# Kernel optimization log

Measured on AMD Instinct MI355X. Metric: run time of the kernel, lower is better.

Reference implementation:

```python
import jax, jax.numpy as jnp
import numpy as np

INPUT_SIZE = 350   # (133 + 42) * 2
HIDDEN = 2048

def setup_inputs() -> dict:
    key = jax.random.key(0)
    ks = jax.random.split(key, 11)
    s = 0.02
    H4 = 4 * HIDDEN
    return {
        "x":     jax.random.normal(ks[0], (1, 133, 2), jnp.float32),
        "W_ih0": jax.random.normal(ks[1], (H4, INPUT_SIZE), jnp.float32) * s,
        "W_hh0": jax.random.normal(ks[2], (H4, HIDDEN), jnp.float32) * s,
        "b_ih0": jax.random.normal(ks[3], (H4,), jnp.float32) * s,
        "b_hh0": jax.random.normal(ks[4], (H4,), jnp.float32) * s,
        "W_ih1": jax.random.normal(ks[5], (H4, HIDDEN), jnp.float32) * s,
        "W_hh1": jax.random.normal(ks[6], (H4, HIDDEN), jnp.float32) * s,
        "b_ih1": jax.random.normal(ks[7], (H4,), jnp.float32) * s,
        "b_hh1": jax.random.normal(ks[8], (H4,), jnp.float32) * s,
        "fc_w":  jax.random.normal(ks[9], (INPUT_SIZE, HIDDEN), jnp.float32) * s,
        "fc_b":  jax.random.normal(ks[10], (INPUT_SIZE,), jnp.float32) * s,
    }

def _prepare(x):
    kp = x[0].astype(jnp.float32)                 # [133, 2]
    src_body, src_face = kp[0], kp[53]
    src_left, src_right = kp[100], kp[121]
    body = kp[:17] - src_body
    feet = kp[17:23]                              # never recentered in original
    face = kp[23:91] - src_face
    l0, r0 = kp[91:112], kp[112:133]
    # bounding-box scales computed BEFORE recentering (matches torch order)
    wl = l0[:, 0].max() - l0[:, 0].min(); hl = l0[:, 1].max() - l0[:, 1].min()
    wr = r0[:, 0].max() - r0[:, 0].min(); hr = r0[:, 1].max() - r0[:, 1].min()
    chin2l = l0 - src_body
    chin2r = r0 - src_body
    left = l0 - src_left
    right = r0 - src_right
    okl = (wl != 0.0) & (hl != 0.0)
    okr = (wr != 0.0) & (hr != 0.0)
    dl = jnp.where(okl, jnp.stack([wl, hl]), jnp.ones(2, kp.dtype))
    dr = jnp.where(okr, jnp.stack([wr, hr]), jnp.ones(2, kp.dtype))
    left = left / dl
    right = right / dr
    return jnp.concatenate([body, feet, face, left, right, chin2l, chin2r]).reshape(INPUT_SIZE)

def _lstm_cell(xin, h, c, Wih, Whh, bih, bhh):
    g = Wih @ xin + bih + Whh @ h + bhh           # [4H]
    i, f, gg, o = jnp.split(g, 4)                 # PyTorch gate order i,f,g,o
    c_new = jax.nn.sigmoid(f) * c + jax.nn.sigmoid(i) * jnp.tanh(gg)
    h_new = jax.nn.sigmoid(o) * jnp.tanh(c_new)
    return h_new, c_new

def reference(x, W_ih0, W_hh0, b_ih0, b_hh0, W_ih1, W_hh1, b_ih1, b_hh1, fc_w, fc_b):
    feat = _prepare(x)                            # [350]
    h0 = jnp.zeros(HIDDEN, feat.dtype)            # initialize_cell_and_hidden_state
    c0 = jnp.zeros(HIDDEN, feat.dtype)
    h1, _ = _lstm_cell(feat, h0, c0, W_ih0, W_hh0, b_ih0, b_hh0)
    h2, _ = _lstm_cell(h1, h0, c0, W_ih1, W_hh1, b_ih1, b_hh1)
    return (fc_w @ h2 + fc_b)[None, :]            # [1, 350]
```

## Files before the change

kernel.cpp:

```cpp
#include <hip/hip_runtime.h>
#include <math.h>

#define HIDDEN 2048
#define IN_F 350

__device__ __forceinline__ float sigmoidf_(float v) { return 1.0f / (1.0f + expf(-v)); }

__device__ void compute_feat(const float* __restrict__ x, float* feat) {
    __shared__ float sc[12];
    const int t = threadIdx.x;
    if (t == 0) {
        sc[0] = x[0];   sc[1] = x[1];
        sc[2] = x[106]; sc[3] = x[107];
        sc[4] = x[200]; sc[5] = x[201];
        sc[6] = x[242]; sc[7] = x[243];
        float lminx = x[182], lmaxx = x[182], lminy = x[183], lmaxy = x[183];
        for (int j = 1; j < 21; ++j) {
            float vx = x[182 + 2*j], vy = x[183 + 2*j];
            lminx = fminf(lminx, vx); lmaxx = fmaxf(lmaxx, vx);
            lminy = fminf(lminy, vy); lmaxy = fmaxf(lmaxy, vy);
        }
        float wl = lmaxx - lminx, hl = lmaxy - lminy;
        float rminx = x[224], rmaxx = x[224], rminy = x[225], rmaxy = x[225];
        for (int j = 1; j < 21; ++j) {
            float vx = x[224 + 2*j], vy = x[225 + 2*j];
            rminx = fminf(rminx, vx); rmaxx = fmaxf(rmaxx, vx);
            rminy = fminf(rminy, vy); rmaxy = fmaxf(rmaxy, vy);
        }
        float wr = rmaxx - rminx, hr = rmaxy - rminy;
        bool okl = (wl != 0.0f) && (hl != 0.0f);
        bool okr = (wr != 0.0f) && (hr != 0.0f);
        sc[8]  = okl ? wl : 1.0f;  sc[9]  = okl ? hl : 1.0f;
        sc[10] = okr ? wr : 1.0f;  sc[11] = okr ? hr : 1.0f;
    }
    __syncthreads();
    const float sbx = sc[0], sby = sc[1], sfx = sc[2], sfy = sc[3];
    const float slx = sc[4], sly = sc[5], srx = sc[6], sry = sc[7];
    const float dlx = sc[8], dly = sc[9], drx = sc[10], dry = sc[11];
    for (int k = t; k < 133; k += blockDim.x) {
        float vx = x[2*k], vy = x[2*k + 1];
        if (k < 17) {
            feat[2*k]   = vx - sbx;  feat[2*k+1] = vy - sby;
        } else if (k < 23) {
            feat[2*k]   = vx;        feat[2*k+1] = vy;
        } else if (k < 91) {
            feat[2*k]   = vx - sfx;  feat[2*k+1] = vy - sfy;
        } else if (k < 112) {
            int j = k - 91;
            feat[182 + 2*j] = (vx - slx) / dlx;  feat[183 + 2*j] = (vy - sly) / dly;
            feat[266 + 2*j] = vx - sbx;          feat[267 + 2*j] = vy - sby;
        } else {
            int j = k - 112;
            feat[224 + 2*j] = (vx - srx) / drx;  feat[225 + 2*j] = (vy - sry) / dry;
            feat[308 + 2*j] = vx - sbx;          feat[309 + 2*j] = vy - sby;
        }
    }
    __syncthreads();
}

__global__ __launch_bounds__(192) void lstm0_kernel(
    const float* __restrict__ x, const float* __restrict__ Wih,
    const float* __restrict__ bih, const float* __restrict__ bhh,
    float* __restrict__ h_out)
{
    __shared__ float feat[IN_F];
    __shared__ float gate_s[3];
    compute_feat(x, feat);
    const int j = blockIdx.x;
    const int wave = threadIdx.x >> 6;
    const int lane = threadIdx.x & 63;
    const int gate = (wave == 0) ? 0 : (wave == 1 ? 2 : 3);
    const int row = gate * HIDDEN + j;
    const float* wr = Wih + (size_t)row * IN_F;
    float acc = 0.0f;
    for (int i = lane; i < IN_F; i += 64) acc += wr[i] * feat[i];
    #pragma unroll
    for (int off = 32; off; off >>= 1) acc += __shfl_down(acc, off);
    if (lane == 0) gate_s[wave] = acc + bih[row] + bhh[row];
    __syncthreads();
    if (threadIdx.x == 0) {
        float c = sigmoidf_(gate_s[0]) * tanhf(gate_s[1]);
        h_out[j] = sigmoidf_(gate_s[2]) * tanhf(c);
    }
}

__global__ __launch_bounds__(192) void lstm1_kernel(
    const float* __restrict__ h_in, const float* __restrict__ Wih,
    const float* __restrict__ bih, const float* __restrict__ bhh,
    float* __restrict__ h_out)
{
    __shared__ float gate_s[3];
    const int j = blockIdx.x;
    const int wave = threadIdx.x >> 6;
    const int lane = threadIdx.x & 63;
    const int gate = (wave == 0) ? 0 : (wave == 1 ? 2 : 3);
    const int row = gate * HIDDEN + j;
    const float4* wr4 = (const float4*)(Wih + (size_t)row * HIDDEN);
    const float4* h4  = (const float4*)h_in;
    float acc = 0.0f;
    #pragma unroll
    for (int i = lane; i < HIDDEN / 4; i += 64) {
        float4 w = wr4[i]; float4 v = h4[i];
        acc += w.x * v.x + w.y * v.y + w.z * v.z + w.w * v.w;
    }
    #pragma unroll
    for (int off = 32; off; off >>= 1) acc += __shfl_down(acc, off);
    if (lane == 0) gate_s[wave] = acc + bih[row] + bhh[row];
    __syncthreads();
    if (threadIdx.x == 0) {
        float c = sigmoidf_(gate_s[0]) * tanhf(gate_s[1]);
        h_out[j] = sigmoidf_(gate_s[2]) * tanhf(c);
    }
}

__global__ __launch_bounds__(256) void fc_kernel(
    const float* __restrict__ h_in, const float* __restrict__ W,
    const float* __restrict__ b, float* __restrict__ out)
{
    const int wave = threadIdx.x >> 6;
    const int lane = threadIdx.x & 63;
    const int r = blockIdx.x * 4 + wave;
    if (r >= IN_F) return;
    const float4* wr4 = (const float4*)(W + (size_t)r * HIDDEN);
    const float4* h4  = (const float4*)h_in;
    float acc = 0.0f;
    #pragma unroll
    for (int i = lane; i < HIDDEN / 4; i += 64) {
        float4 w = wr4[i]; float4 v = h4[i];
        acc += w.x * v.x + w.y * v.y + w.z * v.z + w.w * v.w;
    }
    #pragma unroll
    for (int off = 32; off; off >>= 1) acc += __shfl_down(acc, off);
    if (lane == 0) out[r] = acc + b[r];
}

extern "C" void kernel_launch(void* const* d_in, const int* in_sizes, int n_in,
                              void* d_out, int out_size, void* d_ws, size_t ws_size,
                              hipStream_t stream) {
    const float* x     = (const float*)d_in[0];
    const float* W_ih0 = (const float*)d_in[1];
    const float* b_ih0 = (const float*)d_in[3];
    const float* b_hh0 = (const float*)d_in[4];
    const float* W_ih1 = (const float*)d_in[5];
    const float* b_ih1 = (const float*)d_in[7];
    const float* b_hh1 = (const float*)d_in[8];
    const float* fc_w  = (const float*)d_in[9];
    const float* fc_b  = (const float*)d_in[10];

    float* ws = (float*)d_ws;
    float* h1 = ws;
    float* h2 = ws + HIDDEN;

    lstm0_kernel<<<HIDDEN, 192, 0, stream>>>(x, W_ih0, b_ih0, b_hh0, h1);
    lstm1_kernel<<<HIDDEN, 192, 0, stream>>>(h1, W_ih1, b_ih1, b_hh1, h2);
    fc_kernel<<<(IN_F + 3) / 4, 256, 0, stream>>>(h2, fc_w, fc_b, (float*)d_out);
}
```

Before: 22.88 us.

## Parallelize feature prep, unroll GEMV loads, split FC rows across waves

Feature preparation now spreads the hand bounding-box min/max across several threads using shared staging, instead of a serial scan on thread 0. The LSTM0 GEMV is rewritten as fixed float2 loads, and LSTM1 issues all eight float4 weight loads up front to raise memory-level parallelism. The FC kernel now uses one block per output row with four waves splitting the K dimension, which raises the block count from 88 to 350 at the cost of an extra shared-memory reduction and barrier. The float2 loads in LSTM0 assume 8-byte alignment of rows of length 350, which holds because 350 is even.

```diff
diff --git a/kernel.cpp b/kernel.cpp
--- a/kernel.cpp
+++ b/kernel.cpp
@@ -5,39 +5,53 @@
 #define IN_F 350
 
 __device__ __forceinline__ float sigmoidf_(float v) { return 1.0f / (1.0f + expf(-v)); }
+__device__ __forceinline__ float dot4_(float4 a, float4 b) {
+    return a.x*b.x + a.y*b.y + a.z*b.z + a.w*b.w;
+}
 
-__device__ void compute_feat(const float* __restrict__ x, float* feat) {
+__global__ __launch_bounds__(192) void k1_feat_lstm0(
+    const float* __restrict__ x, const float* __restrict__ Wih,
+    const float* __restrict__ bih, const float* __restrict__ bhh,
+    float* __restrict__ h1)
+{
+    __shared__ __align__(16) float feat[IN_F];
+    __shared__ float hx[84];
     __shared__ float sc[12];
-    const int t = threadIdx.x;
-    if (t == 0) {
-        sc[0] = x[0];   sc[1] = x[1];
-        sc[2] = x[106]; sc[3] = x[107];
-        sc[4] = x[200]; sc[5] = x[201];
-        sc[6] = x[242]; sc[7] = x[243];
-        float lminx = x[182], lmaxx = x[182], lminy = x[183], lmaxy = x[183];
-        for (int j = 1; j < 21; ++j) {
-            float vx = x[182 + 2*j], vy = x[183 + 2*j];
-            lminx = fminf(lminx, vx); lmaxx = fmaxf(lmaxx, vx);
-            lminy = fminf(lminy, vy); lmaxy = fmaxf(lmaxy, vy);
-        }
-        float wl = lmaxx - lminx, hl = lmaxy - lminy;
-        float rminx = x[224], rmaxx = x[224], rminy = x[225], rmaxy = x[225];
-        for (int j = 1; j < 21; ++j) {
-            float vx = x[224 + 2*j], vy = x[225 + 2*j];
-            rminx = fminf(rminx, vx); rmaxx = fmaxf(rmaxx, vx);
-            rminy = fminf(rminy, vy); rmaxy = fmaxf(rmaxy, vy);
-        }
-        float wr = rmaxx - rminx, hr = rmaxy - rminy;
-        bool okl = (wl != 0.0f) && (hl != 0.0f);
-        bool okr = (wr != 0.0f) && (hr != 0.0f);
-        sc[8]  = okl ? wl : 1.0f;  sc[9]  = okl ? hl : 1.0f;
-        sc[10] = okr ? wr : 1.0f;  sc[11] = okr ? hr : 1.0f;
+    __shared__ float ext[4];
+    __shared__ float gd[3];
+    const int tid = threadIdx.x, wave = tid >> 6, lane = tid & 63;
+    const int j = blockIdx.x;
+
+    if (tid < 84) hx[tid] = x[182 + tid];
+    else if (tid < 92) {
+        int t = tid - 84;
+        int p = t >> 1;
+        int base = (p == 0) ? 0 : (p == 1) ? 106 : (p == 2) ? 200 : 242;
+        sc[t] = x[base + (t & 1)];
     }
     __syncthreads();
-    const float sbx = sc[0], sby = sc[1], sfx = sc[2], sfy = sc[3];
-    const float slx = sc[4], sly = sc[5], srx = sc[6], sry = sc[7];
-    const float dlx = sc[8], dly = sc[9], drx = sc[10], dry = sc[11];
-    for (int k = t; k < 133; k += blockDim.x) {
+    if (tid < 4) {
+        const int h = tid >> 1, c = tid & 1;
+        float m = hx[h*42 + c], M = m;
+        #pragma unroll
+        for (int jj = 1; jj < 21; ++jj) {
+            float v = hx[h*42 + 2*jj + c];
+            m = fminf(m, v); M = fmaxf(M, v);
+        }
+        ext[tid] = M - m;
+    }
+    __syncthreads();
+    if (tid < 4) {
+        const int h = tid >> 1;
+        bool ok = (ext[2*h] != 0.0f) && (ext[2*h + 1] != 0.0f);
+        sc[8 + tid] = ok ? ext[tid] : 1.0f;
+    }
+    __syncthreads();
+    if (tid < 133) {
+        const float sbx = sc[0], sby = sc[1], sfx = sc[2], sfy = sc[3];
+        const float slx = sc[4], sly = sc[5], srx = sc[6], sry = sc[7];
+        const float dlx = sc[8], dly = sc[9], drx = sc[10], dry = sc[11];
+        const int k = tid;
         float vx = x[2*k], vy = x[2*k + 1];
         if (k < 17) {
             feat[2*k]   = vx - sbx;  feat[2*k+1] = vy - sby;
@@ -46,92 +60,97 @@
         } else if (k < 91) {
             feat[2*k]   = vx - sfx;  feat[2*k+1] = vy - sfy;
         } else if (k < 112) {
-            int j = k - 91;
-            feat[182 + 2*j] = (vx - slx) / dlx;  feat[183 + 2*j] = (vy - sly) / dly;
-            feat[266 + 2*j] = vx - sbx;          feat[267 + 2*j] = vy - sby;
+            int jj = k - 91;
+            feat[182 + 2*jj] = (vx - slx) / dlx;  feat[183 + 2*jj] = (vy - sly) / dly;
+            feat[266 + 2*jj] = vx - sbx;          feat[267 + 2*jj] = vy - sby;
         } else {
-            int j = k - 112;
-            feat[224 + 2*j] = (vx - srx) / drx;  feat[225 + 2*j] = (vy - sry) / dry;
-            feat[308 + 2*j] = vx - sbx;          feat[309 + 2*j] = vy - sby;
+            int jj = k - 112;
+            feat[224 + 2*jj] = (vx - srx) / drx;  feat[225 + 2*jj] = (vy - sry) / dry;
+            feat[308 + 2*jj] = vx - sbx;          feat[309 + 2*jj] = vy - sby;
         }
     }
     __syncthreads();
-}
 
-__global__ __launch_bounds__(192) void lstm0_kernel(
-    const float* __restrict__ x, const float* __restrict__ Wih,
-    const float* __restrict__ bih, const float* __restrict__ bhh,
-    float* __restrict__ h_out)
-{
-    __shared__ float feat[IN_F];
-    __shared__ float gate_s[3];
-    compute_feat(x, feat);
-    const int j = blockIdx.x;
-    const int wave = threadIdx.x >> 6;
-    const int lane = threadIdx.x & 63;
-    const int gate = (wave == 0) ? 0 : (wave == 1 ? 2 : 3);
-    const int row = gate * HIDDEN + j;
-    const float* wr = Wih + (size_t)row * IN_F;
-    float acc = 0.0f;
-    for (int i = lane; i < IN_F; i += 64) acc += wr[i] * feat[i];
+    const int grow = ((wave == 0) ? 0 : (wave == 1) ? 2 : 3) * HIDDEN + j;
+    const float2* wr = (const float2*)(Wih + (size_t)grow * IN_F);
+    const float2* f2 = (const float2*)feat;
+    const bool has2 = (128 + lane) < 175;
+    float2 w0 = wr[lane];
+    float2 w1 = wr[64 + lane];
+    float2 w2 = has2 ? wr[128 + lane] : make_float2(0.f, 0.f);
+    float2 f0 = f2[lane];
+    float2 f1 = f2[64 + lane];
+    float2 fx = has2 ? f2[128 + lane] : make_float2(0.f, 0.f);
+    float acc = w0.x*f0.x + w0.y*f0.y + w1.x*f1.x + w1.y*f1.y + w2.x*fx.x + w2.y*fx.y;
     #pragma unroll
     for (int off = 32; off; off >>= 1) acc += __shfl_down(acc, off);
-    if (lane == 0) gate_s[wave] = acc + bih[row] + bhh[row];
+    if (lane == 0) gd[wave] = acc + bih[grow] + bhh[grow];
     __syncthreads();
-    if (threadIdx.x == 0) {
-        float c = sigmoidf_(gate_s[0]) * tanhf(gate_s[1]);
-        h_out[j] = sigmoidf_(gate_s[2]) * tanhf(c);
+    if (tid == 0) {
+        float c = sigmoidf_(gd[0]) * tanhf(gd[1]);
+        h1[j] = sigmoidf_(gd[2]) * tanhf(c);
     }
 }
 
-__global__ __launch_bounds__(192) void lstm1_kernel(
-    const float* __restrict__ h_in, const float* __restrict__ Wih,
-    const float* __restrict__ bih, const float* __restrict__ bhh,
-    float* __restrict__ h_out)
+__global__ __launch_bounds__(192) void k2_lstm1(
+    const float* __restrict__ Wih, const float* __restrict__ bih,
+    const float* __restrict__ bhh, const float* __restrict__ h1,
+    float* __restrict__ h2)
 {
-    __shared__ float gate_s[3];
+    __shared__ float gd[3];
+    const int tid = threadIdx.x, wave = tid >> 6, lane = tid & 63;
     const int j = blockIdx.x;
-    const int wave = threadIdx.x >> 6;
-    const int lane = threadIdx.x & 63;
-    const int gate = (wave == 0) ? 0 : (wave == 1 ? 2 : 3);
-    const int row = gate * HIDDEN + j;
-    const float4* wr4 = (const float4*)(Wih + (size_t)row * HIDDEN);
-    const float4* h4  = (const float4*)h_in;
-    float acc = 0.0f;
-    #pragma unroll
-    for (int i = lane; i < HIDDEN / 4; i += 64) {
-        float4 w = wr4[i]; float4 v = h4[i];
-        acc += w.x * v.x + w.y * v.y + w.z * v.z + w.w * v.w;
-    }
+    const int grow = ((wave == 0) ? 0 : (wave == 1) ? 2 : 3) * HIDDEN + j;
+    const float4* wr = (const float4*)(Wih + (size_t)grow * HIDDEN);
+    const float4* h4 = (const float4*)h1;
+
+    float4 wv0 = wr[lane];
+    float4 wv1 = wr[ 64 + lane];
+    float4 wv2 = wr[128 + lane];
+    float4 wv3 = wr[192 + lane];
+    float4 wv4 = wr[256 + lane];
+    float4 wv5 = wr[320 + lane];
+    float4 wv6 = wr[384 + lane];
+    float4 wv7 = wr[448 + lane];
+    float4 hv0 = h4[lane];
+    float4 hv1 = h4[ 64 + lane];
+    float4 hv2 = h4[128 + lane];
+    float4 hv3 = h4[192 + lane];
+    float4 hv4 = h4[256 + lane];
+    float4 hv5 = h4[320 + lane];
+    float4 hv6 = h4[384 + lane];
+    float4 hv7 = h4[448 + lane];
+
+    float acc = dot4_(wv0, hv0) + dot4_(wv1, hv1) + dot4_(wv2, hv2) + dot4_(wv3, hv3)
+              + dot4_(wv4, hv4) + dot4_(wv5, hv5) + dot4_(wv6, hv6) + dot4_(wv7, hv7);
     #pragma unroll
     for (int off = 32; off; off >>= 1) acc += __shfl_down(acc, off);
-    if (lane == 0) gate_s[wave] = acc + bih[row] + bhh[row];
+    if (lane == 0) gd[wave] = acc + bih[grow] + bhh[grow];
     __syncthreads();
-    if (threadIdx.x == 0) {
-        float c = sigmoidf_(gate_s[0]) * tanhf(gate_s[1]);
-        h_out[j] = sigmoidf_(gate_s[2]) * tanhf(c);
+    if (tid == 0) {
+        float c = sigmoidf_(gd[0]) * tanhf(gd[1]);
+        h2[j] = sigmoidf_(gd[2]) * tanhf(c);
     }
 }
 
-__global__ __launch_bounds__(256) void fc_kernel(
-    const float* __restrict__ h_in, const float* __restrict__ W,
+__global__ __launch_bounds__(256) void k3_fc(
+    const float* __restrict__ h2, const float* __restrict__ W,
     const float* __restrict__ b, float* __restrict__ out)
 {
-    const int wave = threadIdx.x >> 6;
-    const int lane = threadIdx.x & 63;
-    const int r = blockIdx.x * 4 + wave;
-    if (r >= IN_F) return;
-    const float4* wr4 = (const float4*)(W + (size_t)r * HIDDEN);
-    const float4* h4  = (const float4*)h_in;
-    float acc = 0.0f;
-    #pragma unroll
-    for (int i = lane; i < HIDDEN / 4; i += 64) {
-        float4 w = wr4[i]; float4 v = h4[i];
-        acc += w.x * v.x + w.y * v.y + w.z * v.z + w.w * v.w;
-    }
+    __shared__ float part[4];
+    const int tid = threadIdx.x, wave = tid >> 6, lane = tid & 63;
+    const int r = blockIdx.x;
+    const float4* wr = (const float4*)(W + (size_t)r * HIDDEN);
+    const float4* h4 = (const float4*)h2;
+    const int base = wave * 128;
+    float4 w0 = wr[base + lane], w1 = wr[base + 64 + lane];
+    float4 v0 = h4[base + lane], v1 = h4[base + 64 + lane];
+    float acc = dot4_(w0, v0) + dot4_(w1, v1);
     #pragma unroll
     for (int off = 32; off; off >>= 1) acc += __shfl_down(acc, off);
-    if (lane == 0) out[r] = acc + b[r];
+    if (lane == 0) part[wave] = acc;
+    __syncthreads();
+    if (tid == 0) out[r] = part[0] + part[1] + part[2] + part[3] + b[r];
 }
 
 extern "C" void kernel_launch(void* const* d_in, const int* in_sizes, int n_in,
@@ -147,11 +166,10 @@
     const float* fc_w  = (const float*)d_in[9];
     const float* fc_b  = (const float*)d_in[10];
 
-    float* ws = (float*)d_ws;
-    float* h1 = ws;
-    float* h2 = ws + HIDDEN;
+    float* h1 = (float*)d_ws;
+    float* h2 = (float*)d_ws + HIDDEN;
 
-    lstm0_kernel<<<HIDDEN, 192, 0, stream>>>(x, W_ih0, b_ih0, b_hh0, h1);
-    lstm1_kernel<<<HIDDEN, 192, 0, stream>>>(h1, W_ih1, b_ih1, b_hh1, h2);
-    fc_kernel<<<(IN_F + 3) / 4, 256, 0, stream>>>(h2, fc_w, fc_b, (float*)d_out);
+    k1_feat_lstm0<<<HIDDEN, 192, 0, stream>>>(x, W_ih0, b_ih0, b_hh0, h1);
+    k2_lstm1<<<HIDDEN, 192, 0, stream>>>(W_ih1, b_ih1, b_hh1, h1, h2);
+    k3_fc<<<IN_F, 256, 0, stream>>>(h2, fc_w, fc_b, (float*)d_out);
 }
```

Result: faster. 21.87 us (-4.5%).
